# Optimization experiments

Measured on AMD Instinct MI355X. Metric: run time of the kernel, lower is better.

Reference implementation:

```python
import jax, jax.numpy as jnp
from jax import lax
import numpy as np

EPS_LN = 1e-5
EPS_BN = 1e-5


def _forward(x, prior, alpha, in_proj_w, conv_w, conv_b, x_proj_weight,
             dt_projs_weight, dt_projs_bias, A_logs, Ds, out_norm_w, out_norm_b,
             out_proj_w, p2w_w1, p2w_b1, p2w_bn_w, p2w_bn_b, p2w_bn_mean,
             p2w_bn_var, p2w_w2, p2w_b2):
    Din = conv_w.shape[0]
    # in_proj (Linear2d == 1x1 conv), split into ssm branch and gate z
    xz = jnp.einsum('bchw,dc->bdhw', x, in_proj_w)          # [B, 2*Din, H, W]
    x_ssm, z = jnp.split(xz, 2, axis=1)
    # depthwise 3x3 conv + SiLU
    x_ssm = lax.conv_general_dilated(
        x_ssm, conv_w, (1, 1), 'SAME',
        dimension_numbers=('NCHW', 'OIHW', 'NCHW'),
        feature_group_count=Din) + conv_b[None, :, None, None]
    x_ssm = jax.nn.silu(x_ssm)

    B, D, H, W = x_ssm.shape
    L = H * W
    K = 4
    R = dt_projs_weight.shape[2]
    N = A_logs.shape[1]

    # cross_scan: 4 directions = row-major, col-major, and their reverses
    row = x_ssm.reshape(B, D, L)
    col = x_ssm.transpose(0, 1, 3, 2).reshape(B, D, L)
    xs = jnp.stack([row, col, row[..., ::-1], col[..., ::-1]], axis=1)  # [B,K,D,L]

    x_dbl = jnp.einsum('bkdl,kcd->bkcl', xs, x_proj_weight)  # [B,K,R+2N,L]
    dts, Bs, Cs = jnp.split(x_dbl, [R, R + N], axis=2)       # [B,K,R,L],[B,K,N,L],[B,K,N,L]
    dts = jnp.einsum('bkrl,kdr->bkdl', dts, dt_projs_weight)  # [B,K,D,L]

    A = -jnp.exp(A_logs.astype(jnp.float32)).reshape(K, D, N)
    dt = jax.nn.softplus(dts + dt_projs_bias[None, :, :, None])  # [B,K,D,L]

    dA = jnp.exp(dt[..., None] * A[None, :, :, None, :])          # [B,K,D,L,N]
    dBx = dt[..., None] * Bs.transpose(0, 1, 3, 2)[:, :, None, :, :] * xs[..., None]
    Cseq = Cs.transpose(0, 1, 3, 2)                               # [B,K,L,N]

    dA_t = jnp.moveaxis(dA, 3, 0)    # [L,B,K,D,N]
    dBx_t = jnp.moveaxis(dBx, 3, 0)  # [L,B,K,D,N]
    C_t = jnp.moveaxis(Cseq, 2, 0)   # [L,B,K,N]

    def step(h, inp):
        a, bx, c = inp
        h = h * a + bx                              # [B,K,D,N]
        y = jnp.einsum('bkdn,bkn->bkd', h, c)
        return h, y

    h0 = jnp.zeros((B, K, D, N), dtype=jnp.float32)
    _, ys = lax.scan(step, h0, (dA_t, dBx_t, C_t))  # [L,B,K,D]
    ys = jnp.moveaxis(ys, 0, 3)                     # [B,K,D,L]
    ys = ys + Ds.reshape(K, D)[None, :, :, None] * xs
    ys = ys.reshape(B, K, D, H, W)

    # prior -> per-direction guidance weights (PriorToWeights, BN in eval mode)
    g = jnp.einsum('bchw,oc->bohw', prior, p2w_w1) + p2w_b1[None, :, None, None]
    g = (g - p2w_bn_mean[None, :, None, None]) * jax.lax.rsqrt(
        p2w_bn_var[None, :, None, None] + EPS_BN)
    g = g * p2w_bn_w[None, :, None, None] + p2w_bn_b[None, :, None, None]
    g = jax.nn.relu(g)
    g = jnp.einsum('bchw,oc->bohw', g, p2w_w2) + p2w_b2[None, :, None, None]
    gw = jax.nn.sigmoid(g)                          # [B,4,H,W]
    s = jax.nn.sigmoid(alpha)                       # [1]
    Wdir = 1.0 + s * (gw - 1.0)                     # torch.lerp(ones, gw, s)
    ys = ys * Wdir[:, :, None, :, :]

    # cross_merge: inverse of cross_scan, sum of 4 directions
    ysl = ys.reshape(B, K, D, L)
    y = ysl[:, 0] + ysl[:, 2, :, ::-1]
    yt = ysl[:, 1] + ysl[:, 3, :, ::-1]
    y = y + yt.reshape(B, D, W, H).transpose(0, 1, 3, 2).reshape(B, D, L)
    y = y.reshape(B, D, H, W)

    # LayerNorm2d: normalize over channel dim
    mu = y.mean(axis=1, keepdims=True)
    var = y.var(axis=1, keepdims=True)
    y = (y - mu) * jax.lax.rsqrt(var + EPS_LN)
    y = y * out_norm_w[None, :, None, None] + out_norm_b[None, :, None, None]

    y = y * jax.nn.silu(z)
    out = jnp.einsum('bdhw,md->bmhw', y, out_proj_w)  # out_proj 1x1, no bias
    return out


def setup_inputs() -> dict:
    key = jax.random.key(0)
    ks = jax.random.split(key, 16)
    B, Dm, H, W = 8, 96, 64, 64
    Din, N, K, R, hid = 192, 1, 4, 6, 32

    def rn(k, shape, scale):
        return jax.random.normal(k, shape, jnp.float32) * scale

    return {
        'x': rn(ks[0], (B, Dm, H, W), 1.0),
        'prior': jax.random.uniform(ks[1], (B, 4, H, W), jnp.float32),
        'alpha': rn(ks[2], (1,), 1.0),
        'in_proj_w': rn(ks[3], (2 * Din, Dm), Dm ** -0.5),
        'conv_w': rn(ks[4], (Din, 1, 3, 3), 1.0 / 3.0),
        'conv_b': rn(ks[5], (Din,), 0.1),
        'x_proj_weight': rn(ks[6], (K, R + 2 * N, Din), Din ** -0.5),
        'dt_projs_weight': rn(ks[7], (K, Din, R), R ** -0.5),
        'dt_projs_bias': rn(ks[8], (K, Din), 0.5) - 4.0,
        'A_logs': jnp.tile(jnp.log(jnp.arange(1, N + 1, dtype=jnp.float32)), (K * Din, 1)),
        'Ds': jnp.ones((K * Din,), jnp.float32),
        'out_norm_w': jnp.ones((Din,), jnp.float32),
        'out_norm_b': jnp.zeros((Din,), jnp.float32),
        'out_proj_w': rn(ks[9], (Dm, Din), Din ** -0.5),
        'p2w_w1': rn(ks[10], (hid, 4), 0.5),
        'p2w_b1': jnp.zeros((hid,), jnp.float32),
        'p2w_bn_w': jnp.ones((hid,), jnp.float32),
        'p2w_bn_b': jnp.zeros((hid,), jnp.float32),
        'p2w_bn_mean': jnp.zeros((hid,), jnp.float32),
        'p2w_bn_var': jnp.ones((hid,), jnp.float32),
        'p2w_w2': rn(ks[11], (4, hid), hid ** -0.5),
        'p2w_b2': jnp.zeros((4,), jnp.float32),
    }


def reference(x, prior, alpha, in_proj_w, conv_w, conv_b, x_proj_weight,
              dt_projs_weight, dt_projs_bias, A_logs, Ds, out_norm_w, out_norm_b,
              out_proj_w, p2w_w1, p2w_b1, p2w_bn_w, p2w_bn_b, p2w_bn_mean,
              p2w_bn_var, p2w_w2, p2w_b2):
    return _forward(x, prior, alpha, in_proj_w, conv_w, conv_b, x_proj_weight,
                    dt_projs_weight, dt_projs_bias, A_logs, Ds, out_norm_w,
                    out_norm_b, out_proj_w, p2w_w1, p2w_b1, p2w_bn_w, p2w_bn_b,
                    p2w_bn_mean, p2w_bn_var, p2w_w2, p2w_b2)
```

## Files before the change

kernel.cpp:

```cpp
#include <hip/hip_runtime.h>

#define BB   8
#define CIN  96
#define DIN  192
#define HH   64
#define WW   64
#define LL   4096
#define KK   4
#define COUT 96
#define SS   128
#define LC   32

#define LOG2E 1.4426950408889634f
#define LN2   0.6931471805599453f

typedef unsigned short bf16t;
typedef float f32x2 __attribute__((ext_vector_type(2)));
typedef float f32x4 __attribute__((ext_vector_type(4)));
typedef short bf16x8s __attribute__((ext_vector_type(8)));

__device__ __forceinline__ f32x2 pkfma(f32x2 a, f32x2 b, f32x2 c) {
#if __has_builtin(__builtin_elementwise_fma)
  return __builtin_elementwise_fma(a, b, c);
#else
  f32x2 r;
  r[0] = fmaf(a[0], b[0], c[0]);
  r[1] = fmaf(a[1], b[1], c[1]);
  return r;
#endif
}

__device__ __forceinline__ float exp2fast(float x) { return __builtin_amdgcn_exp2f(x); }
__device__ __forceinline__ float log2fast(float x) { return __builtin_amdgcn_logf(x); }
__device__ __forceinline__ float sigf(float x) { return 1.0f / (1.0f + __expf(-x)); }
__device__ __forceinline__ int trp(int p) { return ((p & 63) << 6) | (p >> 6); }
__device__ __forceinline__ int pix_of(int k, int l) {
  if (k == 0) return l;
  if (k == 1) return trp(l);
  if (k == 2) return LL - 1 - l;
  return trp(LL - 1 - l);
}
__device__ __forceinline__ float b2f(bf16t v) {
  return __uint_as_float((unsigned)v << 16);
}
__device__ __forceinline__ bf16t f2b(float f) {
  unsigned u = __float_as_uint(f);
  return (bf16t)((u + 0x7FFFu + ((u >> 16) & 1u)) >> 16);
}

__global__ __launch_bounds__(256) void gemm_in_mfma_k(const float* __restrict__ x,
                                                      const bf16t* __restrict__ Wb,
                                                      bf16t* __restrict__ out) {
  __shared__ bf16t ldsB[32 * 104];
  const int tid = threadIdx.x;
  const int b = blockIdx.z;
  const int p0 = blockIdx.x * 32;
  for (int idx = tid; idx < CIN * 32; idx += 256) {
    int c = idx >> 5, px = idx & 31;
    ldsB[px * 104 + c] = f2b(x[((size_t)b * CIN + c) * LL + p0 + px]);
  }
  __syncthreads();
  const int wave = tid >> 6, lane = tid & 63;
  const int lm = lane & 15, kc = lane >> 4;
  bf16x8s bfrag[2][3];
#pragma unroll
  for (int nf = 0; nf < 2; ++nf)
#pragma unroll
    for (int ks = 0; ks < 3; ++ks)
      bfrag[nf][ks] = *(const bf16x8s*)&ldsB[(nf * 16 + lm) * 104 + ks * 32 + kc * 8];
  bf16t* ob = out + (size_t)b * 384 * LL + p0;
#pragma unroll
  for (int mti = 0; mti < 6; ++mti) {
    const int o0 = (wave * 6 + mti) * 16;
    bf16x8s afrag[3];
#pragma unroll
    for (int ks = 0; ks < 3; ++ks)
      afrag[ks] = *(const bf16x8s*)&Wb[(size_t)(o0 + lm) * CIN + ks * 32 + kc * 8];
    f32x4 acc0 = {0.f, 0.f, 0.f, 0.f};
    f32x4 acc1 = {0.f, 0.f, 0.f, 0.f};
#pragma unroll
    for (int ks = 0; ks < 3; ++ks) {
      acc0 = __builtin_amdgcn_mfma_f32_16x16x32_bf16(afrag[ks], bfrag[0][ks], acc0, 0, 0, 0);
      acc1 = __builtin_amdgcn_mfma_f32_16x16x32_bf16(afrag[ks], bfrag[1][ks], acc1, 0, 0, 0);
    }
#pragma unroll
    for (int r = 0; r < 4; ++r) {
      ob[(size_t)(o0 + kc * 4 + r) * LL + lm]      = f2b(acc0[r]);
      ob[(size_t)(o0 + kc * 4 + r) * LL + 16 + lm] = f2b(acc1[r]);
    }
  }
}

__global__ __launch_bounds__(256) void gemm_out_k(const bf16t* __restrict__ in,
                                                  const float* __restrict__ W,
                                                  float* __restrict__ out) {
  const int tid = threadIdx.x;
  const int b  = blockIdx.z;
  const int o0 = blockIdx.y * 4;
  const int p0 = blockIdx.x * 1024 + tid * 4;
  const bf16t* inb = in + (size_t)b * DIN * LL + p0;
  const float* Wb  = W + (size_t)o0 * DIN;
  f32x2 accL[4], accH[4];
#pragma unroll
  for (int j = 0; j < 4; ++j) { accL[j] = (f32x2){0.f, 0.f}; accH[j] = (f32x2){0.f, 0.f}; }
#pragma unroll 4
  for (int c = 0; c < DIN; c += 4) {
    float4 w[4];
#pragma unroll
    for (int j = 0; j < 4; ++j) w[j] = *(const float4*)&Wb[j * DIN + c];
    f32x2 xlo[4], xhi[4];
#pragma unroll
    for (int t = 0; t < 4; ++t) {
      ushort4 xu = *(const ushort4*)&inb[(size_t)(c + t) * LL];
      xlo[t] = (f32x2){b2f(xu.x), b2f(xu.y)};
      xhi[t] = (f32x2){b2f(xu.z), b2f(xu.w)};
    }
#pragma unroll
    for (int j = 0; j < 4; ++j) {
#pragma unroll
      for (int t = 0; t < 4; ++t) {
        const float ws = t == 0 ? w[j].x : t == 1 ? w[j].y : t == 2 ? w[j].z : w[j].w;
        const f32x2 wv = {ws, ws};
        accL[j] = pkfma(xlo[t], wv, accL[j]);
        accH[j] = pkfma(xhi[t], wv, accH[j]);
      }
    }
  }
  float* ob = out + (size_t)b * COUT * LL + p0;
#pragma unroll
  for (int j = 0; j < 4; ++j) {
    float4 st = make_float4(accL[j][0], accL[j][1], accH[j][0], accH[j][1]);
    *(float4*)&ob[(size_t)(o0 + j) * LL] = st;
  }
}

__global__ __launch_bounds__(256) void p2w_k(const float* __restrict__ prior,
                                             const float* __restrict__ alpha,
                                             const float* __restrict__ w1,
                                             const float* __restrict__ b1,
                                             const float* __restrict__ bnw,
                                             const float* __restrict__ bnb,
                                             const float* __restrict__ bnm,
                                             const float* __restrict__ bnv,
                                             const float* __restrict__ w2,
                                             const float* __restrict__ b2,
                                             const float* __restrict__ xpw,
                                             const float* __restrict__ ipw,
                                             float* __restrict__ xpwT,
                                             bf16t* __restrict__ ipwb,
                                             float* __restrict__ Wg) {
  if (blockIdx.x == 0) {
    for (int idx = threadIdx.x; idx < KK * DIN * 8; idx += 256) {
      int kk = idx / (DIN * 8);
      int rem = idx % (DIN * 8);
      int dd = rem >> 3, c = rem & 7;
      xpwT[idx] = xpw[(kk * 8 + c) * DIN + dd];
    }
  }
  if (blockIdx.x == 1) {
    for (int idx = threadIdx.x; idx < 384 * CIN; idx += 256)
      ipwb[idx] = f2b(ipw[idx]);
  }
  int idx = blockIdx.x * 256 + threadIdx.x;
  int p = idx & (LL - 1);
  int b = idx >> 12;
  float pr[4];
#pragma unroll
  for (int c = 0; c < 4; ++c) pr[c] = prior[((size_t)b * 4 + c) * LL + p];
  float s = sigf(alpha[0]);
  float g2[4];
#pragma unroll
  for (int j = 0; j < 4; ++j) g2[j] = b2[j];
  for (int o = 0; o < 32; ++o) {
    float g = b1[o];
#pragma unroll
    for (int c = 0; c < 4; ++c) g = fmaf(pr[c], w1[o * 4 + c], g);
    g = (g - bnm[o]) * rsqrtf(bnv[o] + 1e-5f) * bnw[o] + bnb[o];
    g = fmaxf(g, 0.0f);
#pragma unroll
    for (int j = 0; j < 4; ++j) g2[j] = fmaf(g, w2[j * 32 + o], g2[j]);
  }
#pragma unroll
  for (int j = 0; j < 4; ++j)
    Wg[((size_t)b * 4 + j) * LL + p] = 1.0f + s * (sigf(g2[j]) - 1.0f);
}

__global__ __launch_bounds__(1024) void convproj_k(const bf16t* __restrict__ xz,
                                                   const float* __restrict__ cw,
                                                   const float* __restrict__ cb,
                                                   const float* __restrict__ xpwT,
                                                   bf16t* __restrict__ xcT,
                                                   float* __restrict__ projS) {
  __shared__ float sX[96 * 65];
  __shared__ float4 sP[512];
  const int tid = threadIdx.x;
  const int b = blockIdx.y;
  const int h = blockIdx.x;
  const int px = tid & 63;
  const int ku = __builtin_amdgcn_readfirstlane((tid >> 6) & 3);
  const int hf = __builtin_amdgcn_readfirstlane((tid >> 8) & 1);
  const int q  = __builtin_amdgcn_readfirstlane(tid >> 9);
  f32x2 a01 = {0.f, 0.f}, a23 = {0.f, 0.f};

#pragma unroll
  for (int half = 0; half < 2; ++half) {
    for (int idx = tid; idx < 96 * 16; idx += 1024) {
      int ddl = idx >> 4, pq = idx & 15;
      int w0 = pq * 4;
      int dd = half * 96 + ddl;
      const bf16t* base = xz + ((size_t)b * 384 + dd) * LL + h * 64 + w0;
      const float* wp = cw + dd * 9;
      float bv = cb[dd];
      f32x2 s01 = {bv, bv}, s23 = {bv, bv};
#pragma unroll
      for (int dh = -1; dh <= 1; ++dh) {
        int hh = h + dh;
        if (hh < 0 || hh >= HH) continue;
        const bf16t* row = base + dh * 64;
        ushort4 cmu = *(const ushort4*)row;
        float cmx = b2f(cmu.x), cmy = b2f(cmu.y), cmz = b2f(cmu.z), cmw = b2f(cmu.w);
        float lf = (w0 > 0)  ? b2f(row[-1]) : 0.0f;
        float rt = (w0 < 60) ? b2f(row[4])  : 0.0f;
        float c0 = wp[(dh + 1) * 3], c1 = wp[(dh + 1) * 3 + 1], c2 = wp[(dh + 1) * 3 + 2];
        s01 = pkfma((f32x2){lf,  cmx}, (f32x2){c0, c0}, s01);
        s01 = pkfma((f32x2){cmx, cmy}, (f32x2){c1, c1}, s01);
        s01 = pkfma((f32x2){cmy, cmz}, (f32x2){c2, c2}, s01);
        s23 = pkfma((f32x2){cmy, cmz}, (f32x2){c0, c0}, s23);
        s23 = pkfma((f32x2){cmz, cmw}, (f32x2){c1, c1}, s23);
        s23 = pkfma((f32x2){cmw, rt},  (f32x2){c2, c2}, s23);
      }
      float* so = &sX[ddl * 65 + w0];
      float v0 = s01[0], v1 = s01[1], v2 = s23[0], v3 = s23[1];
      so[0] = v0 * sigf(v0);
      so[1] = v1 * sigf(v1);
      so[2] = v2 * sigf(v2);
      so[3] = v3 * sigf(v3);
    }
    __syncthreads();
    for (int idx = tid; idx < 64 * 96; idx += 1024) {
      int pp = idx / 96, ddl = idx % 96;
      xcT[((size_t)b * LL + h * 64 + pp) * DIN + half * 96 + ddl] =
          f2b(sX[ddl * 65 + pp]);
    }
    {
      const int ddl0 = q * 48;
      const float* wp = xpwT + (size_t)ku * (DIN * 8) + (half * 96 + ddl0) * 8 + hf * 4;
#pragma unroll 8
      for (int d48 = 0; d48 < 48; ++d48) {
        float xv = sX[(ddl0 + d48) * 65 + px];
        const float4 w4 = *(const float4*)(wp + d48 * 8);
        const f32x2 xv2 = {xv, xv};
        a01 = pkfma(xv2, (f32x2){w4.x, w4.y}, a01);
        a23 = pkfma(xv2, (f32x2){w4.z, w4.w}, a23);
      }
    }
    __syncthreads();
  }
  const int slot = tid & 511;
  if (q == 1) sP[slot] = make_float4(a01[0], a01[1], a23[0], a23[1]);
  __syncthreads();
  if (q == 0) {
    float4 o = sP[slot];
    float r0 = a01[0] + o.x, r1 = a01[1] + o.y, r2 = a23[0] + o.z, r3 = a23[1] + o.w;
    const int p = h * 64 + px;
    int l;
    if (ku == 0) l = p;
    else if (ku == 1) l = trp(p);
    else if (ku == 2) l = LL - 1 - p;
    else l = LL - 1 - trp(p);
    float* pb = projS + (((size_t)b * KK + ku) * LL + l) * 8 + hf * 4;
    *(float4*)pb = make_float4(r0, r1, r2, r3);
  }
}

__global__ __launch_bounds__(192) void scan_part_k(const bf16t* __restrict__ xcT,
                                                   const float* __restrict__ projS,
                                                   const float* __restrict__ dtw,
                                                   const float* __restrict__ dtb,
                                                   const float* __restrict__ A_logs,
                                                   float* __restrict__ carrP,
                                                   float* __restrict__ carrH) {
  const int s = blockIdx.x, kp = blockIdx.y, b = blockIdx.z;
  const int d = threadIdx.x;
  const int kA = kp, kB = kp + 2;
  const int s2 = SS - 1 - s;
  const int kdA = kA * DIN + d, kdB = kB * DIN + d;
  float wrA[6], wrB[6];
#pragma unroll
  for (int r = 0; r < 6; ++r) { wrA[r] = dtw[kdA * 6 + r]; wrB[r] = dtw[kdB * 6 + r]; }
  const float biasA = dtb[kdA], biasB = dtb[kdB];
  const float AaA = -__expf(A_logs[kdA]), AaB = -__expf(A_logs[kdB]);
  const int l0 = s * LC;
  const int p0 = pix_of(kA, l0);
  const int dp = pix_of(kA, l0 + 1) - p0;
  const bf16t* xp = xcT + ((size_t)b * LL + p0) * DIN + d;
  const long xstep = (long)dp * DIN;
  const float* prA = projS + (((size_t)b * KK + kA) * LL + l0) * 8;
  const float* prB = projS + (((size_t)b * KK + kB) * LL + s2 * LC + (LC - 1)) * 8;
  float PA = 1.0f, HA = 0.0f, PB = 1.0f, HB = 0.0f;
#pragma unroll 2
  for (int j = 0; j < LC; ++j) {
    float4 a0 = *(const float4*)prA;
    float4 a1 = *(const float4*)(prA + 4);
    prA += 8;
    float4 b0 = *(const float4*)prB;
    float4 b1 = *(const float4*)(prB + 4);
    prB -= 8;
    float xv = b2f(*xp);
    xp += xstep;
    {
      float dtr = biasA;
      dtr = fmaf(a0.x, wrA[0], dtr);
      dtr = fmaf(a0.y, wrA[1], dtr);
      dtr = fmaf(a0.z, wrA[2], dtr);
      dtr = fmaf(a0.w, wrA[3], dtr);
      dtr = fmaf(a1.x, wrA[4], dtr);
      dtr = fmaf(a1.y, wrA[5], dtr);
      float e = exp2fast(fminf(dtr, 80.0f) * LOG2E);
      float u = log2fast(1.0f + e);
      float a = exp2fast(u * AaA);
      float dt = u * LN2;
      HA = fmaf(a, HA, dt * a1.z * xv);
      PA *= a;
    }
    {
      float dtr = biasB;
      dtr = fmaf(b0.x, wrB[0], dtr);
      dtr = fmaf(b0.y, wrB[1], dtr);
      dtr = fmaf(b0.z, wrB[2], dtr);
      dtr = fmaf(b0.w, wrB[3], dtr);
      dtr = fmaf(b1.x, wrB[4], dtr);
      dtr = fmaf(b1.y, wrB[5], dtr);
      float e = exp2fast(fminf(dtr, 80.0f) * LOG2E);
      float u = log2fast(1.0f + e);
      float a = exp2fast(u * AaB);
      float dt = u * LN2;
      HB = fmaf(PB, dt * b1.z * xv, HB);
      PB *= a;
    }
  }
  size_t oA = ((size_t)((b * KK + kA) * SS + s)) * DIN + d;
  size_t oB = ((size_t)((b * KK + kB) * SS + s2)) * DIN + d;
  carrP[oA] = PA;
  carrH[oA] = HA;
  carrP[oB] = PB;
  carrH[oB] = HB;
}

__global__ __launch_bounds__(192) void scan_fix_k(const float* __restrict__ carrP,
                                                  const float* __restrict__ carrH,
                                                  float* __restrict__ h0) {
  const int k = blockIdx.x, b = blockIdx.y, d = threadIdx.x;
  size_t base = ((size_t)(b * KK + k)) * SS * DIN + d;
  float h = 0.0f;
#pragma unroll 4
  for (int s = 0; s < SS; ++s) {
    h0[base + (size_t)s * DIN] = h;
    h = fmaf(carrP[base + (size_t)s * DIN], h, carrH[base + (size_t)s * DIN]);
  }
}

__global__ __launch_bounds__(192) void scan_apply_k(const bf16t* __restrict__ xcT,
                                                    const float* __restrict__ projS,
                                                    const float* __restrict__ Wg,
                                                    const float* __restrict__ h0,
                                                    const float* __restrict__ dtw,
                                                    const float* __restrict__ dtb,
                                                    const float* __restrict__ A_logs,
                                                    const float* __restrict__ Ds,
                                                    bf16t* __restrict__ ymT,
                                                    bf16t* __restrict__ ymT2) {
  const int s = blockIdx.x, kp = blockIdx.y, b = blockIdx.z;
  const int d = threadIdx.x;
  __shared__ float sAcc[LC * DIN];
  float xr[LC];
  {
    const int k = kp, kd = k * DIN + d;
    float wr[6];
#pragma unroll
    for (int r = 0; r < 6; ++r) wr[r] = dtw[kd * 6 + r];
    const float bias = dtb[kd];
    const float Aa = -__expf(A_logs[kd]);
    const float Dv = Ds[kd];
    const int l0 = s * LC;
    const int p0 = pix_of(k, l0);
    const int dp = pix_of(k, l0 + 1) - p0;
    const bf16t* xp = xcT + ((size_t)b * LL + p0) * DIN + d;
    const long xstep = (long)dp * DIN;
    const float* pr = projS + (((size_t)b * KK + k) * LL + l0) * 8;
    const float* wg = Wg + ((size_t)b * KK + k) * LL + l0;
    float h = h0[((size_t)((b * KK + k) * SS + s)) * DIN + d];
#pragma unroll
    for (int j = 0; j < LC; ++j) {
      float4 q0 = *(const float4*)pr;
      float4 q1 = *(const float4*)(pr + 4);
      pr += 8;
      float xv = b2f(*xp);
      xp += xstep;
      xr[j] = xv;
      float dtr = bias;
      dtr = fmaf(q0.x, wr[0], dtr);
      dtr = fmaf(q0.y, wr[1], dtr);
      dtr = fmaf(q0.z, wr[2], dtr);
      dtr = fmaf(q0.w, wr[3], dtr);
      dtr = fmaf(q1.x, wr[4], dtr);
      dtr = fmaf(q1.y, wr[5], dtr);
      float e = exp2fast(fminf(dtr, 80.0f) * LOG2E);
      float u = log2fast(1.0f + e);
      float a = exp2fast(u * Aa);
      float dt = u * LN2;
      h = fmaf(a, h, dt * q1.z * xv);
      sAcc[j * DIN + d] = fmaf(h, q1.w, Dv * xv) * wg[j];
    }
  }
  {
    const int k = kp + 2, kd = k * DIN + d;
    const int s2 = SS - 1 - s;
    float wr[6];
#pragma unroll
    for (int r = 0; r < 6; ++r) wr[r] = dtw[kd * 6 + r];
    const float bias = dtb[kd];
    const float Aa = -__expf(A_logs[kd]);
    const float Dv = Ds[kd];
    const int l0 = s2 * LC;
    const float* pr = projS + (((size_t)b * KK + k) * LL + l0) * 8;
    const float* wg = Wg + ((size_t)b * KK + k) * LL + l0;
    float h = h0[((size_t)((b * KK + k) * SS + s2)) * DIN + d];
#pragma unroll
    for (int j = 0; j < LC; ++j) {
      float4 q0 = *(const float4*)pr;
      float4 q1 = *(const float4*)(pr + 4);
      pr += 8;
      float xv = xr[LC - 1 - j];
      float dtr = bias;
      dtr = fmaf(q0.x, wr[0], dtr);
      dtr = fmaf(q0.y, wr[1], dtr);
      dtr = fmaf(q0.z, wr[2], dtr);
      dtr = fmaf(q0.w, wr[3], dtr);
      dtr = fmaf(q1.x, wr[4], dtr);
      dtr = fmaf(q1.y, wr[5], dtr);
      float e = exp2fast(fminf(dtr, 80.0f) * LOG2E);
      float u = log2fast(1.0f + e);
      float a = exp2fast(u * Aa);
      float dt = u * LN2;
      h = fmaf(a, h, dt * q1.z * xv);
      float y = fmaf(h, q1.w, Dv * xv) * wg[j];
      sAcc[(LC - 1 - j) * DIN + d] += y;
    }
  }
  bf16t* dst;
  if (kp == 0)
    dst = ymT + (size_t)b * (384 * (size_t)LL) + (size_t)(s * LC) * DIN + d;
  else
    dst = ymT2 + ((size_t)b * LL + s * LC) * DIN + d;
#pragma unroll 4
  for (int j = 0; j < LC; ++j) dst[(size_t)j * DIN] = f2b(sAcc[j * DIN + d]);
}

__global__ __launch_bounds__(256) void ln_silu_k(const bf16t* __restrict__ ymT,
                                                 const bf16t* __restrict__ ymT2,
                                                 const bf16t* __restrict__ xz,
                                                 const float* __restrict__ gamma,
                                                 const float* __restrict__ beta,
                                                 bf16t* __restrict__ u) {
  const int b = blockIdx.y;
  const int h = blockIdx.x;
  const int p0 = h * 64;
  __shared__ float sY[64 * 193];
  __shared__ float sS[4][64], sQ[4][64];
  const int tid = threadIdx.x;
  const bf16t* ymb = ymT + (size_t)b * (384 * (size_t)LL);
  for (int idx = tid; idx < 64 * DIN; idx += 256) {
    int pp = idx / DIN, dd = idx % DIN;
    float v = b2f(ymb[(size_t)(p0 + pp) * DIN + dd]) +
              b2f(ymT2[((size_t)b * LL + pp * 64 + h) * DIN + dd]);
    sY[pp * 193 + dd] = v;
  }
  __syncthreads();
  const int px = tid & 63, g = tid >> 6;
  float sum = 0.0f, ss = 0.0f;
  for (int dd = g * 48; dd < g * 48 + 48; ++dd) {
    float v = sY[px * 193 + dd];
    sum += v;
    ss = fmaf(v, v, ss);
  }
  sS[g][px] = sum;
  sQ[g][px] = ss;
  __syncthreads();
  sum = sS[0][px] + sS[1][px] + sS[2][px] + sS[3][px];
  ss  = sQ[0][px] + sQ[1][px] + sQ[2][px] + sQ[3][px];
  const float mu = sum * (1.0f / DIN);
  float var = ss * (1.0f / DIN) - mu * mu;
  const float rstd = rsqrtf(fmaxf(var, 0.0f) + 1e-5f);
  const bf16t* zb = xz + ((size_t)b * 384 + DIN) * LL + p0 + px;
  bf16t* ub = u + (size_t)b * DIN * LL + p0 + px;
  for (int dd = g * 48; dd < g * 48 + 48; ++dd) {
    float v = sY[px * 193 + dd];
    float z = b2f(zb[(size_t)dd * LL]);
    float tn = fmaf((v - mu) * rstd, gamma[dd], beta[dd]);
    ub[(size_t)dd * LL] = f2b(tn * (z * sigf(z)));
  }
}

extern "C" void kernel_launch(void* const* d_in, const int* in_sizes, int n_in,
                              void* d_out, int out_size, void* d_ws, size_t ws_size,
                              hipStream_t stream) {
  const float* x      = (const float*)d_in[0];
  const float* prior  = (const float*)d_in[1];
  const float* alpha  = (const float*)d_in[2];
  const float* ipw    = (const float*)d_in[3];
  const float* cw     = (const float*)d_in[4];
  const float* cb     = (const float*)d_in[5];
  const float* xpw    = (const float*)d_in[6];
  const float* dtw    = (const float*)d_in[7];
  const float* dtb    = (const float*)d_in[8];
  const float* A_logs = (const float*)d_in[9];
  const float* Ds     = (const float*)d_in[10];
  const float* onw    = (const float*)d_in[11];
  const float* onb    = (const float*)d_in[12];
  const float* opw    = (const float*)d_in[13];
  const float* w1     = (const float*)d_in[14];
  const float* b1     = (const float*)d_in[15];
  const float* bnw    = (const float*)d_in[16];
  const float* bnb    = (const float*)d_in[17];
  const float* bnm    = (const float*)d_in[18];
  const float* bnv    = (const float*)d_in[19];
  const float* w2     = (const float*)d_in[20];
  const float* b2     = (const float*)d_in[21];
  float* out = (float*)d_out;

  char* ws = (char*)d_ws;
  bf16t* xz    = (bf16t*)(ws);
  bf16t* xcT   = (bf16t*)(ws + 25165824);
  bf16t* ymT2  = (bf16t*)(ws + 37748736);
  float* projS = (float*)(ws + 50331648);
  float* Wgb   = (float*)(ws + 54525952);
  float* carrP = (float*)(ws + 55050240);
  float* carrH = (float*)(ws + 58195968);
  float* h0b   = (float*)(ws + 61341696);
  float* xpwT  = (float*)(ws + 64487424);
  bf16t* ipwb  = (bf16t*)(ws + 64512000);
  bf16t* ymT   = xz;
  bf16t* u     = xcT;

  p2w_k<<<(BB * LL) / 256, 256, 0, stream>>>(prior, alpha, w1, b1, bnw, bnb, bnm,
                                             bnv, w2, b2, xpw, ipw, xpwT, ipwb, Wgb);
  gemm_in_mfma_k<<<dim3(LL / 32, 1, BB), 256, 0, stream>>>(x, ipwb, xz);
  convproj_k<<<dim3(HH, BB), 1024, 0, stream>>>(xz, cw, cb, xpwT, xcT, projS);
  scan_part_k<<<dim3(SS, 2, BB), 192, 0, stream>>>(xcT, projS, dtw, dtb, A_logs,
                                                   carrP, carrH);
  scan_fix_k<<<dim3(KK, BB), 192, 0, stream>>>(carrP, carrH, h0b);
  scan_apply_k<<<dim3(SS, 2, BB), 192, 0, stream>>>(xcT, projS, Wgb, h0b, dtw, dtb,
                                                    A_logs, Ds, ymT, ymT2);
  ln_silu_k<<<dim3(HH, BB), 256, 0, stream>>>(ymT, ymT2, xz, onw, onb, u);
  gemm_out_k<<<dim3(LL / 1024, COUT / 4, BB), 256, 0, stream>>>(u, opw, out);
}
```

Before: 174.6 us.

## Replace scalar output projection with bf16 MFMA using split hi/lo weights

The output projection GEMM moves from packed-FMA scalar code to MFMA bf16 instructions. The fp32 weights are pre-split into high and low bf16 parts in the prep kernel, so precision stays close to fp32 on the weight side. Activation tiles are staged transposed in LDS with padding. This cuts ALU work but does two MFMAs per k-step, and the LDS transpose store may cause bank conflicts.

```diff
diff --git a/kernel.cpp b/kernel.cpp
--- a/kernel.cpp
+++ b/kernel.cpp
@@ -91,46 +91,41 @@
   }
 }
 
-__global__ __launch_bounds__(256) void gemm_out_k(const bf16t* __restrict__ in,
-                                                  const float* __restrict__ W,
-                                                  float* __restrict__ out) {
+__global__ __launch_bounds__(384) void gemm_out_mfma_k(const bf16t* __restrict__ u,
+                                                       const bf16t* __restrict__ Wh,
+                                                       const bf16t* __restrict__ Wl,
+                                                       float* __restrict__ out) {
+  __shared__ bf16t ldsB[64 * 200];
   const int tid = threadIdx.x;
-  const int b  = blockIdx.z;
-  const int o0 = blockIdx.y * 4;
-  const int p0 = blockIdx.x * 1024 + tid * 4;
-  const bf16t* inb = in + (size_t)b * DIN * LL + p0;
-  const float* Wb  = W + (size_t)o0 * DIN;
-  f32x2 accL[4], accH[4];
-#pragma unroll
-  for (int j = 0; j < 4; ++j) { accL[j] = (f32x2){0.f, 0.f}; accH[j] = (f32x2){0.f, 0.f}; }
-#pragma unroll 4
-  for (int c = 0; c < DIN; c += 4) {
-    float4 w[4];
-#pragma unroll
-    for (int j = 0; j < 4; ++j) w[j] = *(const float4*)&Wb[j * DIN + c];
-    f32x2 xlo[4], xhi[4];
-#pragma unroll
-    for (int t = 0; t < 4; ++t) {
-      ushort4 xu = *(const ushort4*)&inb[(size_t)(c + t) * LL];
-      xlo[t] = (f32x2){b2f(xu.x), b2f(xu.y)};
-      xhi[t] = (f32x2){b2f(xu.z), b2f(xu.w)};
-    }
-#pragma unroll
-    for (int j = 0; j < 4; ++j) {
-#pragma unroll
-      for (int t = 0; t < 4; ++t) {
-        const float ws = t == 0 ? w[j].x : t == 1 ? w[j].y : t == 2 ? w[j].z : w[j].w;
-        const f32x2 wv = {ws, ws};
-        accL[j] = pkfma(xlo[t], wv, accL[j]);
-        accH[j] = pkfma(xhi[t], wv, accH[j]);
-      }
-    }
+  const int b = blockIdx.z;
+  const int p0 = blockIdx.x * 64;
+  for (int idx = tid; idx < DIN * 64; idx += 384) {
+    int c = idx >> 6, px = idx & 63;
+    ldsB[px * 200 + c] = u[((size_t)b * DIN + c) * LL + p0 + px];
+  }
+  __syncthreads();
+  const int wave = tid / 64, lane = tid & 63;
+  const int lm = lane & 15, kc = lane >> 4;
+  const int o0 = wave * 16;
+  bf16x8s ah[6], al[6];
+#pragma unroll
+  for (int ks = 0; ks < 6; ++ks) {
+    ah[ks] = *(const bf16x8s*)&Wh[(size_t)(o0 + lm) * DIN + ks * 32 + kc * 8];
+    al[ks] = *(const bf16x8s*)&Wl[(size_t)(o0 + lm) * DIN + ks * 32 + kc * 8];
   }
   float* ob = out + (size_t)b * COUT * LL + p0;
 #pragma unroll
-  for (int j = 0; j < 4; ++j) {
-    float4 st = make_float4(accL[j][0], accL[j][1], accH[j][0], accH[j][1]);
-    *(float4*)&ob[(size_t)(o0 + j) * LL] = st;
+  for (int nf = 0; nf < 4; ++nf) {
+    f32x4 acc = {0.f, 0.f, 0.f, 0.f};
+#pragma unroll
+    for (int ks = 0; ks < 6; ++ks) {
+      bf16x8s bfr = *(const bf16x8s*)&ldsB[(nf * 16 + lm) * 200 + ks * 32 + kc * 8];
+      acc = __builtin_amdgcn_mfma_f32_16x16x32_bf16(ah[ks], bfr, acc, 0, 0, 0);
+      acc = __builtin_amdgcn_mfma_f32_16x16x32_bf16(al[ks], bfr, acc, 0, 0, 0);
+    }
+#pragma unroll
+    for (int r = 0; r < 4; ++r)
+      ob[(size_t)(o0 + kc * 4 + r) * LL + nf * 16 + lm] = acc[r];
   }
 }
 
@@ -146,8 +141,11 @@
                                              const float* __restrict__ b2,
                                              const float* __restrict__ xpw,
                                              const float* __restrict__ ipw,
+                                             const float* __restrict__ opw,
                                              float* __restrict__ xpwT,
                                              bf16t* __restrict__ ipwb,
+                                             bf16t* __restrict__ opwbh,
+                                             bf16t* __restrict__ opwbl,
                                              float* __restrict__ Wg) {
   if (blockIdx.x == 0) {
     for (int idx = threadIdx.x; idx < KK * DIN * 8; idx += 256) {
@@ -160,6 +158,14 @@
   if (blockIdx.x == 1) {
     for (int idx = threadIdx.x; idx < 384 * CIN; idx += 256)
       ipwb[idx] = f2b(ipw[idx]);
+  }
+  if (blockIdx.x == 2) {
+    for (int idx = threadIdx.x; idx < COUT * DIN; idx += 256) {
+      float w = opw[idx];
+      bf16t hi = f2b(w);
+      opwbh[idx] = hi;
+      opwbl[idx] = f2b(w - b2f(hi));
+    }
   }
   int idx = blockIdx.x * 256 + threadIdx.x;
   int p = idx & (LL - 1);
@@ -540,11 +546,14 @@
   float* h0b   = (float*)(ws + 61341696);
   float* xpwT  = (float*)(ws + 64487424);
   bf16t* ipwb  = (bf16t*)(ws + 64512000);
+  bf16t* opwbh = (bf16t*)(ws + 64585728);
+  bf16t* opwbl = (bf16t*)(ws + 64622592);
   bf16t* ymT   = xz;
   bf16t* u     = xcT;
 
   p2w_k<<<(BB * LL) / 256, 256, 0, stream>>>(prior, alpha, w1, b1, bnw, bnb, bnm,
-                                             bnv, w2, b2, xpw, ipw, xpwT, ipwb, Wgb);
+                                             bnv, w2, b2, xpw, ipw, opw, xpwT,
+                                             ipwb, opwbh, opwbl, Wgb);
   gemm_in_mfma_k<<<dim3(LL / 32, 1, BB), 256, 0, stream>>>(x, ipwb, xz);
   convproj_k<<<dim3(HH, BB), 1024, 0, stream>>>(xz, cw, cb, xpwT, xcT, projS);
   scan_part_k<<<dim3(SS, 2, BB), 192, 0, stream>>>(xcT, projS, dtw, dtb, A_logs,
@@ -553,5 +562,5 @@
   scan_apply_k<<<dim3(SS, 2, BB), 192, 0, stream>>>(xcT, projS, Wgb, h0b, dtw, dtb,
                                                     A_logs, Ds, ymT, ymT2);
   ln_silu_k<<<dim3(HH, BB), 256, 0, stream>>>(ymT, ymT2, xz, onw, onb, u);
-  gemm_out_k<<<dim3(LL / 1024, COUT / 4, BB), 256, 0, stream>>>(u, opw, out);
-}
+  gemm_out_mfma_k<<<dim3(LL / 64, 1, BB), 384, 0, stream>>>(u, opwbh, opwbl, out);
+}
```

Result: faster. 162.4 us (-7.0%).
